# Performance work log

Hardware: AMD Instinct MI355X
Metric: run time of the kernel (lower is better)

Reference implementation:

```python
import jax, jax.numpy as jnp
import numpy as np

IOU_THRESHOLD = 0.1
N_DETS = 8192


def setup_inputs() -> dict:
    key = jax.random.key(0)
    k1, k2, k3 = jax.random.split(key, 3)
    cxcy = jax.random.uniform(k1, (N_DETS, 2)) * jnp.array([1920.0, 1080.0])
    wh = 10.0 + jax.random.uniform(k2, (N_DETS, 2)) * 70.0
    bboxes_cxcywh = jnp.concatenate([cxcy, wh], axis=-1).astype(jnp.float32)
    conf = jax.random.uniform(k3, (N_DETS,), dtype=jnp.float32)
    return {"bboxes_cxcywh": bboxes_cxcywh, "conf": conf}


def _box_iou(b):
    # cxcywh -> xyxy (torchvision.ops.box_convert)
    cx, cy, w, h = b[:, 0], b[:, 1], b[:, 2], b[:, 3]
    x1, y1 = cx - 0.5 * w, cy - 0.5 * h
    x2, y2 = cx + 0.5 * w, cy + 0.5 * h
    boxes = jnp.stack([x1, y1, x2, y2], axis=-1)  # [N,4]
    area = (x2 - x1) * (y2 - y1)  # [N]
    lt = jnp.maximum(boxes[:, None, :2], boxes[None, :, :2])  # [N,N,2]
    rb = jnp.minimum(boxes[:, None, 2:], boxes[None, :, 2:])  # [N,N,2]
    iwh = jnp.clip(rb - lt, 0.0)
    inter = iwh[..., 0] * iwh[..., 1]  # [N,N]
    return inter / (area[:, None] + area[None, :] - inter)


def _cluster(iou, conf):
    # Faithful replication of the sequential double loop:
    #   for i: for j>i: if iou[i,j]>thr: a[i]=a[j]=min(a[i],a[j])
    # For fixed i the inner loop is a masked running-min over j (a[i] only
    # decreases), so each row is one vectorized cummin; rows stay sequential
    # via lax.scan (this single pass is NOT full connected components).
    N = iou.shape[0]
    idx = jnp.arange(N, dtype=jnp.int32)

    def body(a, xs):
        i, row = xs
        edge = (row > IOU_THRESHOLD) & (idx > i)
        vals = jnp.where(edge, a, N)  # N = sentinel > any label
        run = jnp.minimum(jax.lax.cummin(vals), a[i])  # running min incl a[i]
        a = jnp.where(edge, run, a)
        a = a.at[i].set(run[-1])  # final a[i] (unchanged if no edges)
        return a, None

    a, _ = jax.lax.scan(body, idx, (idx, iou))

    # relabel unique cluster ids to 0..K-1 (rank of label among present labels)
    present = jnp.zeros(N, jnp.int32).at[a].set(1)
    seg = (jnp.cumsum(present) - 1)[a]  # [N] in [0,K)

    BIG = N
    counts = jnp.zeros(N, jnp.int32).at[seg].add(1)
    # singleton cluster: representative is the member's original index
    single_idx = jnp.full(N, BIG, jnp.int32).at[seg].min(idx)
    # multi-member cluster (faithful to torch code, incl. its subset-index
    # quirk): argmax of conf[members] -> position WITHIN the sorted subset
    maxconf = jnp.full(N, -jnp.inf, conf.dtype).at[seg].max(conf)
    cand = jnp.where(conf == maxconf[seg], idx, BIG)
    g = jnp.full(N, BIG, jnp.int32).at[seg].min(cand)  # first global argmax per cluster
    order = jnp.argsort(seg)  # stable
    starts = jnp.cumsum(counts) - counts
    rank = jnp.zeros(N, jnp.int32).at[order].set(idx - starts[seg[order]])
    pos = rank[jnp.minimum(g, N - 1)]  # within-subset position of argmax
    reprs = jnp.where(counts == 1, single_idx, pos)
    scatter_idx = jnp.where(counts > 0, reprs, BIG)  # invalid clusters dropped
    mask = jnp.zeros(N, bool).at[scatter_idx].set(True, mode='drop')
    return seg, mask


def reference(bboxes_cxcywh, conf):
    iou = _box_iou(bboxes_cxcywh)
    _, mask = _cluster(iou, conf)
    return mask  # return_mode='mask'
```

## Files before the change

kernel.cpp:

```cpp
#include <hip/hip_runtime.h>
#include <stdint.h>

#define NDET 8192
#define ROWCAP 128
#define BATCH 256
#define NBATCH (NDET / BATCH)


#define EW(e) ((e) < 8 ? (((e) >> 1) == 0 ? pa.x : ((e) >> 1) == 1 ? pa.y : ((e) >> 1) == 2 ? pa.z : pa.w) \
                       : ((((e) - 8) >> 1) == 0 ? pb.x : (((e) - 8) >> 1) == 1 ? pb.y : (((e) - 8) >> 1) == 2 ? pb.z : pb.w))
#define EDGE(e) ((int)((EW(e) >> (((e) & 1) * 16)) & 0xFFFFu))

__device__ __forceinline__ void box_corners(const float4 b, float& x1, float& y1,
                                            float& x2, float& y2, float& ar) {
  #pragma clang fp contract(off)
  x1 = b.x - 0.5f * b.z; y1 = b.y - 0.5f * b.w;
  x2 = b.x + 0.5f * b.z; y2 = b.y + 0.5f * b.w;
  ar = (x2 - x1) * (y2 - y1);
}

__global__ __launch_bounds__(256) void k_edges(const float4* __restrict__ bb,
    uint32_t* __restrict__ cnt, uint16_t* __restrict__ edges) {
  #pragma clang fp contract(off)
  int wid  = (blockIdx.x * 256 + threadIdx.x) >> 6;
  int lane = threadIdx.x & 63;
  for (int half = 0; half < 2; ++half) {
    int r = (half == 0) ? wid : (NDET - 1 - wid);
    float ix1, iy1, ix2, iy2, ai;
    box_corners(bb[r], ix1, iy1, ix2, iy2, ai);
    uint16_t* erow = edges + (size_t)r * ROWCAP;
    int cnt_total = 0;
    for (int jc = (r + 1) >> 6; jc < NDET / 64; ++jc) {
      int j = (jc << 6) + lane;
      bool pred = false;
      if (j > r) {
        float jx1, jy1, jx2, jy2, aj;
        box_corners(bb[j], jx1, jy1, jx2, jy2, aj);
        float ltx = fmaxf(ix1, jx1), lty = fmaxf(iy1, jy1);
        float rbx = fminf(ix2, jx2), rby = fminf(iy2, jy2);
        float iw = fmaxf(rbx - ltx, 0.0f), ih = fmaxf(rby - lty, 0.0f);
        float inter = iw * ih;
        float uni = ai + aj - inter;
        float iou = inter / uni;
        pred = iou > 0.1f;
      }
      unsigned long long m = __ballot(pred);
      if (pred) {
        int pos = cnt_total + __popcll(m & ((1ull << lane) - 1ull));
        if (pos < ROWCAP) erow[pos] = (uint16_t)j;
      }
      cnt_total += __popcll(m);
    }
    if (lane == 0) cnt[r] = (uint32_t)min(cnt_total, ROWCAP);
  }
}

__global__ __launch_bounds__(256) void k_sched(const uint16_t* __restrict__ edges,
    const uint32_t* __restrict__ cnt, uint16_t* __restrict__ sched,
    int* __restrict__ depth, uint32_t* __restrict__ minidx,
    unsigned long long* __restrict__ mcg, uint32_t* __restrict__ cntk,
    uint32_t* __restrict__ rankk) {
  __shared__ uint32_t claim[NDET];
  __shared__ int nleft;
  const int t = threadIdx.x;
  const int base = blockIdx.x << 8;
  const int r = base + t;
  minidx[r] = 0xFFFFFFFFu;
  mcg[r] = 0ull; cntk[r] = 0u; rankk[r] = 0u;
  {
    uint4* c4 = reinterpret_cast<uint4*>(claim);
    uint4 ff = make_uint4(0xFFFFFFFFu, 0xFFFFFFFFu, 0xFFFFFFFFu, 0xFFFFFFFFu);
    for (int v = t; v < NDET / 4; v += 256) c4[v] = ff;
  }
  const uint16_t* ep = edges + (size_t)r * ROWCAP;
  uint4 pa = *reinterpret_cast<const uint4*>(ep);
  uint4 pb = *reinterpret_cast<const uint4*>(ep + 8);
  uint32_t deg = cnt[r];
  int js[16];
  #pragma unroll
  for (int e = 0; e < 16; ++e) js[e] = EDGE(e);
  if (t == 0) nleft = 0;
  __syncthreads();
  bool done = (deg == 0u);
  if (!done) atomicAdd(&nleft, 1);
  uint32_t myround = 0u;
  int k = 0;
  __syncthreads();

  while (nleft > 0) {
    ++k;
    const uint32_t key = ((uint32_t)(600 - k) << 9) | (uint32_t)t;
    if (!done) {
      atomicMin(&claim[r], key);
      #pragma unroll
      for (int e = 0; e < 16; ++e)
        if (e < (int)deg) atomicMin(&claim[js[e]], key);
      if (deg > 16u)
        for (int e = 16; e < (int)deg; ++e) atomicMin(&claim[(int)ep[e]], key);
    }
    __syncthreads();
    if (!done) {
      uint32_t cl[16];
      #pragma unroll
      for (int e = 0; e < 16; ++e)
        cl[e] = (e < (int)deg) ? claim[js[e]] : key;
      bool ready = (claim[r] == key);
      #pragma unroll
      for (int e = 0; e < 16; ++e)
        if (cl[e] != key) ready = false;
      if (ready && deg > 16u)
        for (int e = 16; ready && e < (int)deg; ++e)
          if (claim[(int)ep[e]] != key) ready = false;
      if (ready) { myround = (uint32_t)k; done = true; atomicSub(&nleft, 1); }
    }
    __syncthreads();
  }
  sched[r] = (uint16_t)myround;
  if (t == 0) depth[blockIdx.x] = k;
}

__global__ __launch_bounds__(256) void k_scan(const uint16_t* __restrict__ edges,
    const uint32_t* __restrict__ cnt, const uint16_t* __restrict__ sched,
    const int* __restrict__ depth, const float* __restrict__ conf,
    unsigned long long* __restrict__ mcg, uint32_t* __restrict__ cntk,
    uint32_t* __restrict__ rankk, uint32_t* __restrict__ minidx,
    int32_t* __restrict__ out) {
  __shared__ uint16_t a[NDET];
  const int t = threadIdx.x;
  for (int v = t; v < NDET; v += 256) a[v] = (uint16_t)v;

  const uint16_t* ep = edges + (size_t)t * ROWCAP;
  uint4 pa = *reinterpret_cast<const uint4*>(ep);
  uint4 pb = *reinterpret_cast<const uint4*>(ep + 8);
  uint32_t deg = cnt[t];
  uint32_t rnd = sched[t];
  int dep = depth[0];
  __syncthreads();

  for (int b = 0; b < NBATCH; ++b) {
    const int r = (b << 8) + t;
    uint4 pan = make_uint4(0, 0, 0, 0), pbn = make_uint4(0, 0, 0, 0);
    uint32_t degn = 0u, rndn = 0u;
    int depn = 0;
    if (b < NBATCH - 1) {
      const uint16_t* en = edges + (size_t)(r + BATCH) * ROWCAP;
      pan = *reinterpret_cast<const uint4*>(en);
      pbn = *reinterpret_cast<const uint4*>(en + 8);
      degn = cnt[r + BATCH];
      rndn = sched[r + BATCH];
      depn = depth[b + 1];
    }
    for (int k = 1; k <= dep; ++k) {
      if (rnd == (uint32_t)k) {
        int js[16], ls[16];
        #pragma unroll
        for (int e = 0; e < 16; ++e) js[e] = EDGE(e);
        #pragma unroll
        for (int e = 0; e < 16; ++e)
          ls[e] = (e < (int)deg) ? (int)a[js[e]] : 0x7FFFFFFF;
        int cur = (int)a[r];
        #pragma unroll
        for (int e = 0; e < 16; ++e) {
          if (ls[e] < cur) cur = ls[e];
          ls[e] = cur;
        }
        #pragma unroll
        for (int e = 0; e < 16; ++e)
          if (e < (int)deg) a[js[e]] = (uint16_t)ls[e];
        if (deg > 16u) {
          for (int e = 16; e < (int)deg; ++e) {
            int j = (int)edges[(size_t)r * ROWCAP + e];
            int aj = (int)a[j];
            if (aj < cur) cur = aj;
            a[j] = (uint16_t)cur;
          }
        }
        a[r] = (uint16_t)cur;
      }
      __syncthreads();
    }
    pa = pan; pb = pbn; deg = degn; rnd = rndn; dep = depn;
  }
  for (int v = t; v < NDET; v += 256) {
    out[v] = 0;
    uint32_t L = (uint32_t)a[v];
    unsigned long long key = ((unsigned long long)__float_as_uint(conf[v]) << 32)
                           | (unsigned long long)(NDET - 1 - v);
    atomicMax(&mcg[L], key);
    atomicAdd(&cntk[L], 1u);
    atomicMin(&minidx[L], (uint32_t)v);
  }
  __syncthreads(); __threadfence();
  for (int v = t; v < NDET; v += 256) {
    uint32_t L = (uint32_t)a[v];
    uint32_t g = (uint32_t)(NDET - 1) - (uint32_t)(mcg[L] & 0xFFFFFFFFull);
    if ((uint32_t)v < g) atomicAdd(&rankk[L], 1u);
  }
  __syncthreads(); __threadfence();
  for (int L = t; L < NDET; L += 256) {
    uint32_t c = cntk[L];
    if (c > 0u) {
      uint32_t idx = (c == 1u) ? minidx[L] : rankk[L];
      out[idx] = 1;
    }
  }
}

extern "C" void kernel_launch(void* const* d_in, const int* in_sizes, int n_in,
                              void* d_out, int out_size, void* d_ws, size_t ws_size,
                              hipStream_t stream) {
  const float4* bb  = (const float4*)d_in[0];
  const float* conf = (const float*)d_in[1];
  char* ws = (char*)d_ws;
  uint32_t*           cnt    = (uint32_t*)(ws + 0);
  unsigned long long* mcg    = (unsigned long long*)(ws + 65536);
  uint32_t*           cntk   = (uint32_t*)(ws + 131072);
  uint32_t*           rankk  = (uint32_t*)(ws + 163840);
  uint32_t*           minidx = (uint32_t*)(ws + 196608);
  uint16_t*           sched  = (uint16_t*)(ws + 229376);
  int*                depth  = (int*)(ws + 245760);
  uint16_t*           edges  = (uint16_t*)(ws + 262144);
  int32_t* out = (int32_t*)d_out;

  hipLaunchKernelGGL(k_edges, dim3(1024),   dim3(256), 0, stream,
                     bb, cnt, edges);
  hipLaunchKernelGGL(k_sched, dim3(NBATCH), dim3(256), 0, stream,
                     edges, cnt, sched, depth, minidx, mcg, cntk, rankk);
  hipLaunchKernelGGL(k_scan,  dim3(1),      dim3(256), 0, stream,
                     edges, cnt, sched, depth, conf, mcg, cntk, rankk, minidx, out);
}
```

Measured before the change: 338.5 us.

## Shrink scan batch to one wavefront and move cluster fold to LDS kernel

```diff
diff --git a/kernel.cpp b/kernel.cpp
--- a/kernel.cpp
+++ b/kernel.cpp
@@ -3,7 +3,7 @@
 
 #define NDET 8192
 #define ROWCAP 128
-#define BATCH 256
+#define BATCH 64
 #define NBATCH (NDET / BATCH)
 
 
@@ -55,22 +55,17 @@
   }
 }
 
-__global__ __launch_bounds__(256) void k_sched(const uint16_t* __restrict__ edges,
+__global__ __launch_bounds__(64) void k_sched(const uint16_t* __restrict__ edges,
     const uint32_t* __restrict__ cnt, uint16_t* __restrict__ sched,
-    int* __restrict__ depth, uint32_t* __restrict__ minidx,
-    unsigned long long* __restrict__ mcg, uint32_t* __restrict__ cntk,
-    uint32_t* __restrict__ rankk) {
+    int* __restrict__ depth) {
   __shared__ uint32_t claim[NDET];
   __shared__ int nleft;
   const int t = threadIdx.x;
-  const int base = blockIdx.x << 8;
-  const int r = base + t;
-  minidx[r] = 0xFFFFFFFFu;
-  mcg[r] = 0ull; cntk[r] = 0u; rankk[r] = 0u;
+  const int r = (blockIdx.x << 6) + t;
   {
     uint4* c4 = reinterpret_cast<uint4*>(claim);
     uint4 ff = make_uint4(0xFFFFFFFFu, 0xFFFFFFFFu, 0xFFFFFFFFu, 0xFFFFFFFFu);
-    for (int v = t; v < NDET / 4; v += 256) c4[v] = ff;
+    for (int v = t; v < NDET / 4; v += 64) c4[v] = ff;
   }
   const uint16_t* ep = edges + (size_t)r * ROWCAP;
   uint4 pa = *reinterpret_cast<const uint4*>(ep);
@@ -119,15 +114,12 @@
   if (t == 0) depth[blockIdx.x] = k;
 }
 
-__global__ __launch_bounds__(256) void k_scan(const uint16_t* __restrict__ edges,
+__global__ __launch_bounds__(64) void k_scan(const uint16_t* __restrict__ edges,
     const uint32_t* __restrict__ cnt, const uint16_t* __restrict__ sched,
-    const int* __restrict__ depth, const float* __restrict__ conf,
-    unsigned long long* __restrict__ mcg, uint32_t* __restrict__ cntk,
-    uint32_t* __restrict__ rankk, uint32_t* __restrict__ minidx,
-    int32_t* __restrict__ out) {
+    const int* __restrict__ depth, uint32_t* __restrict__ alab) {
   __shared__ uint16_t a[NDET];
   const int t = threadIdx.x;
-  for (int v = t; v < NDET; v += 256) a[v] = (uint16_t)v;
+  for (int v = t; v < NDET; v += 64) a[v] = (uint16_t)v;
 
   const uint16_t* ep = edges + (size_t)t * ROWCAP;
   uint4 pa = *reinterpret_cast<const uint4*>(ep);
@@ -138,7 +130,7 @@
   __syncthreads();
 
   for (int b = 0; b < NBATCH; ++b) {
-    const int r = (b << 8) + t;
+    const int r = (b << 6) + t;
     uint4 pan = make_uint4(0, 0, 0, 0), pbn = make_uint4(0, 0, 0, 0);
     uint32_t degn = 0u, rndn = 0u;
     int depn = 0;
@@ -181,26 +173,46 @@
     }
     pa = pan; pb = pbn; deg = degn; rnd = rndn; dep = depn;
   }
-  for (int v = t; v < NDET; v += 256) {
-    out[v] = 0;
-    uint32_t L = (uint32_t)a[v];
-    unsigned long long key = ((unsigned long long)__float_as_uint(conf[v]) << 32)
-                           | (unsigned long long)(NDET - 1 - v);
-    atomicMax(&mcg[L], key);
-    atomicAdd(&cntk[L], 1u);
-    atomicMin(&minidx[L], (uint32_t)v);
-  }
-  __syncthreads(); __threadfence();
-  for (int v = t; v < NDET; v += 256) {
-    uint32_t L = (uint32_t)a[v];
-    uint32_t g = (uint32_t)(NDET - 1) - (uint32_t)(mcg[L] & 0xFFFFFFFFull);
-    if ((uint32_t)v < g) atomicAdd(&rankk[L], 1u);
-  }
-  __syncthreads(); __threadfence();
-  for (int L = t; L < NDET; L += 256) {
-    uint32_t c = cntk[L];
+
+  __syncthreads();
+  for (int v = t; v < NDET; v += 64) alab[v] = (uint32_t)a[v];
+}
+
+__global__ __launch_bounds__(1024) void k_fold(const uint32_t* __restrict__ alab,
+    const float* __restrict__ conf, int32_t* __restrict__ out) {
+  __shared__ uint32_t T1[NDET];
+  __shared__ uint32_t T2[NDET];
+  const int t = threadIdx.x;
+  for (int v = t; v < NDET; v += 1024) { T1[v] = 0u; T2[v] = 0xFFFFFFFFu; out[v] = 0; }
+  __syncthreads();
+  uint32_t L[8], cb[8];
+  #pragma unroll
+  for (int i = 0; i < 8; ++i) {
+    int v = t + i * 1024;
+    L[i]  = alab[v];
+    cb[i] = __float_as_uint(conf[v]);
+    atomicMax(&T1[L[i]], cb[i]);
+  }
+  __syncthreads();
+  #pragma unroll
+  for (int i = 0; i < 8; ++i) {
+    int v = t + i * 1024;
+    if (T1[L[i]] == cb[i]) atomicMin(&T2[L[i]], (uint32_t)v);
+  }
+  __syncthreads();
+  for (int v = t; v < NDET; v += 1024) T1[v] = 0u;
+  __syncthreads();
+  #pragma unroll
+  for (int i = 0; i < 8; ++i) {
+    int v = t + i * 1024;
+    atomicAdd(&T1[L[i]], 1u + (((uint32_t)v < T2[L[i]]) ? 0x10000u : 0u));
+  }
+  __syncthreads();
+  for (int Lv = t; Lv < NDET; Lv += 1024) {
+    uint32_t cr = T1[Lv];
+    uint32_t c  = cr & 0xFFFFu;
     if (c > 0u) {
-      uint32_t idx = (c == 1u) ? minidx[L] : rankk[L];
+      uint32_t idx = (c == 1u) ? T2[Lv] : (cr >> 16);
       out[idx] = 1;
     }
   }
@@ -212,20 +224,15 @@
   const float4* bb  = (const float4*)d_in[0];
   const float* conf = (const float*)d_in[1];
   char* ws = (char*)d_ws;
-  uint32_t*           cnt    = (uint32_t*)(ws + 0);
-  unsigned long long* mcg    = (unsigned long long*)(ws + 65536);
-  uint32_t*           cntk   = (uint32_t*)(ws + 131072);
-  uint32_t*           rankk  = (uint32_t*)(ws + 163840);
-  uint32_t*           minidx = (uint32_t*)(ws + 196608);
-  uint16_t*           sched  = (uint16_t*)(ws + 229376);
-  int*                depth  = (int*)(ws + 245760);
-  uint16_t*           edges  = (uint16_t*)(ws + 262144);
+  uint32_t* cnt   = (uint32_t*)(ws + 0);
+  uint32_t* alab  = (uint32_t*)(ws + 32768);
+  uint16_t* sched = (uint16_t*)(ws + 65536);
+  int*      depth = (int*)(ws + 81920);
+  uint16_t* edges = (uint16_t*)(ws + 131072);
   int32_t* out = (int32_t*)d_out;
 
-  hipLaunchKernelGGL(k_edges, dim3(1024),   dim3(256), 0, stream,
-                     bb, cnt, edges);
-  hipLaunchKernelGGL(k_sched, dim3(NBATCH), dim3(256), 0, stream,
-                     edges, cnt, sched, depth, minidx, mcg, cntk, rankk);
-  hipLaunchKernelGGL(k_scan,  dim3(1),      dim3(256), 0, stream,
-                     edges, cnt, sched, depth, conf, mcg, cntk, rankk, minidx, out);
-}
+  hipLaunchKernelGGL(k_edges, dim3(1024),   dim3(256),  0, stream, bb, cnt, edges);
+  hipLaunchKernelGGL(k_sched, dim3(NBATCH), dim3(64),   0, stream, edges, cnt, sched, depth);
+  hipLaunchKernelGGL(k_scan,  dim3(1),      dim3(64),   0, stream, edges, cnt, sched, depth, alab);
+  hipLaunchKernelGGL(k_fold,  dim3(1),      dim3(1024), 0, stream, alab, conf, out);
+}
```

New measurement: 395.0 us. 1.17x slower.
